# Performance work log

Hardware: AMD Instinct MI355X
Metric: run time of the kernel (lower is better)

## Reference

```python
import jax, jax.numpy as jnp
import numpy as np

N_NODES = 100000


def _gcn_conv(x, edge_index, W, b, n_nodes):
    # GCNConv: add self-loops, symmetric degree normalization, then
    # out[dst] += norm * (x @ W)[src], plus bias.
    src, dst = edge_index[0], edge_index[1]
    loops = jnp.arange(n_nodes, dtype=src.dtype)
    src = jnp.concatenate([src, loops])
    dst = jnp.concatenate([dst, loops])
    deg = jax.ops.segment_sum(jnp.ones_like(dst, dtype=x.dtype), dst,
                              num_segments=n_nodes)
    dinv = jnp.where(deg > 0, jax.lax.rsqrt(deg), 0.0)
    norm = dinv[src] * dinv[dst]            # [E+N]
    h = x @ W                               # [N, out]  (transform BEFORE gather)
    msg = h[src] * norm[:, None]            # [E+N, out]
    out = jax.ops.segment_sum(msg, dst, num_segments=n_nodes)
    return out + b


def setup_inputs() -> dict:
    key = jax.random.key(0)
    ks = jax.random.split(key, 5)
    x = jax.random.normal(ks[0], (N_NODES, 512), dtype=jnp.float32)
    edge_index = jax.random.randint(ks[1], (2, 3200000), 0, N_NODES, dtype=jnp.int64)
    W1 = jax.random.normal(ks[2], (512, 16), dtype=jnp.float32) * (1.0 / np.sqrt(512))
    b1 = jnp.zeros((16,), dtype=jnp.float32)
    W2 = jax.random.normal(ks[3], (16, 7), dtype=jnp.float32) * (1.0 / np.sqrt(16))
    b2 = jnp.zeros((7,), dtype=jnp.float32)
    return {"x": x, "edge_index": edge_index, "W1": W1, "b1": b1, "W2": W2, "b2": b2}


def reference(x, edge_index, W1, b1, W2, b2):
    n = x.shape[0]
    h = _gcn_conv(x, edge_index, W1, b1, n)
    h = jax.nn.relu(h)
    # F.dropout(training=False) is identity in eval mode
    h = _gcn_conv(h, edge_index, W2, b2, n)
    return jax.nn.log_softmax(h, axis=1)
```

## Files before the change

kernel.cpp:

```cpp
#include <hip/hip_runtime.h>
#include <hip/hip_bf16.h>

#define N_NODES 100000
#define N_EDGES 3200000
#define F_IN    512
#define F_H     16
#define F_OUT   7
#define NB      391
#define GPART   512
#define PER_BLK 6256
#define NTILES  6250
#define CAPB    10240
#define NPAD    (NB * 256)

typedef unsigned int u32;
typedef __attribute__((ext_vector_type(8))) __bf16 bf16x8;
typedef __attribute__((ext_vector_type(4))) float f32x4;

union FragU { uint4 q; bf16x8 v; };

static __device__ __forceinline__ float bflo(u32 u) { return __uint_as_float(u << 16); }
static __device__ __forceinline__ float bfhi(u32 u) { return __uint_as_float(u & 0xFFFF0000u); }
static __device__ __forceinline__ unsigned short f2bf(float f) {
  u32 x = __float_as_uint(f);
  x += 0x7FFF + ((x >> 16) & 1);
  return (unsigned short)(x >> 16);
}
static __device__ __forceinline__ u32 cvt2(float a, float b) {
  u32 r;
  asm("v_cvt_pk_bf16_f32 %0, %1, %2" : "=v"(r) : "v"(a), "v"(b));
  return r;
}

__global__ __launch_bounds__(512) void k_prep(int* __restrict__ gcur,
                                              const float* __restrict__ W1,
                                              uint4* __restrict__ bfragG) {
  int tid = threadIdx.x;
  if (tid < NB) gcur[tid] = tid * CAPB;
  for (int idx = tid; idx < 1024; idx += 512) {
    int kk = idx >> 6, lane = idx & 63;
    int col = lane & 15, g = lane >> 4;
    int k0 = kk * 32 + g * 8;
    uint4 q;
    q.x = cvt2(W1[(k0 + 0) * 16 + col], W1[(k0 + 1) * 16 + col]);
    q.y = cvt2(W1[(k0 + 2) * 16 + col], W1[(k0 + 3) * 16 + col]);
    q.z = cvt2(W1[(k0 + 4) * 16 + col], W1[(k0 + 5) * 16 + col]);
    q.w = cvt2(W1[(k0 + 6) * 16 + col], W1[(k0 + 7) * 16 + col]);
    bfragG[idx] = q;
  }
}

__global__ __launch_bounds__(256) void k_part(const int* __restrict__ src,
                                              const int* __restrict__ dst,
                                              int* __restrict__ gcur,
                                              u32* __restrict__ pairs) {
  __shared__ int h[NB];
  __shared__ int lbase[NB];
  __shared__ int lcur[NB];
  int tid = threadIdx.x, blk = blockIdx.x;
  for (int b = tid; b < NB; b += 256) h[b] = 0;
  __syncthreads();
  int e0 = blk * PER_BLK;
  int n = min(PER_BLK, N_EDGES - e0);
  const int4* s4 = (const int4*)(src + e0);
  const int4* d4 = (const int4*)(dst + e0);
  for (int i = tid; i < (n >> 2); i += 256) {
    int4 d = d4[i];
    atomicAdd(&h[d.x >> 8], 1);
    atomicAdd(&h[d.y >> 8], 1);
    atomicAdd(&h[d.z >> 8], 1);
    atomicAdd(&h[d.w >> 8], 1);
  }
  __syncthreads();
  for (int b = tid; b < NB; b += 256) {
    int c = h[b];
    lbase[b] = c ? atomicAdd(&gcur[b], c) : 0;
    lcur[b] = 0;
  }
  __syncthreads();
  for (int i = tid; i < (n >> 2); i += 256) {
    int4 sv = s4[i];
    int4 dv = d4[i];
    { int b = dv.x >> 8; u32 v = ((u32)(dv.x & 255) << 17) | (u32)sv.x;
      pairs[lbase[b] + atomicAdd(&lcur[b], 1)] = v; }
    { int b = dv.y >> 8; u32 v = ((u32)(dv.y & 255) << 17) | (u32)sv.y;
      pairs[lbase[b] + atomicAdd(&lcur[b], 1)] = v; }
    { int b = dv.z >> 8; u32 v = ((u32)(dv.z & 255) << 17) | (u32)sv.z;
      pairs[lbase[b] + atomicAdd(&lcur[b], 1)] = v; }
    { int b = dv.w >> 8; u32 v = ((u32)(dv.w & 255) << 17) | (u32)sv.w;
      pairs[lbase[b] + atomicAdd(&lcur[b], 1)] = v; }
  }
}

__global__ __launch_bounds__(256) void k_deg(const u32* __restrict__ pairs,
                                             const int* __restrict__ gcur,
                                             int* __restrict__ dega,
                                             int* __restrict__ excla) {
  __shared__ int h[256];
  __shared__ int sc[256];
  int tid = threadIdx.x, b = blockIdx.x;
  h[tid] = 0;
  __syncthreads();
  int base = b * CAPB;
  int cnt = gcur[b] - base;
  for (int k = tid; k < cnt; k += 256)
    atomicAdd(&h[pairs[base + k] >> 17], 1);
  __syncthreads();
  int c = h[tid];
  sc[tid] = c;
  __syncthreads();
  for (int off = 1; off < 256; off <<= 1) {
    int v = (tid >= off) ? sc[tid - off] : 0;
    __syncthreads();
    sc[tid] += v;
    __syncthreads();
  }
  int node = b * 256 + tid;
  dega[node] = c;
  excla[node] = sc[tid] - c;
}

__global__ __launch_bounds__(256) void k_gemm1(const float* __restrict__ x,
                                               const uint4* __restrict__ bfragG,
                                               const int* __restrict__ dega,
                                               unsigned short* __restrict__ h1p) {
  __shared__ __align__(16) char ldsbuf[2][64 * 80];
  int tid = threadIdx.x;
  int blockRow0 = blockIdx.x * 64;

  int r0 = tid >> 3, r1 = r0 + 32, s = tid & 7;
  bool ok1 = (blockRow0 + r1) < N_NODES;
  const float* x0 = x + (size_t)(blockRow0 + r0) * F_IN + s * 4;
  const float* x1 = x + (size_t)(blockRow0 + r1) * F_IN + s * 4;

  int wv = tid >> 6, lane = tid & 63;
  int col = lane & 15, g = lane >> 4;
  int wid = blockIdx.x * 4 + wv;
  int fragRow = wv * 16 + col;

  f32x4 acc = {0.f, 0.f, 0.f, 0.f};

  {
    float4 fA = *(const float4*)(x0);
    float4 fB = ok1 ? *(const float4*)(x1) : make_float4(0.f, 0.f, 0.f, 0.f);
    uint2 qA = {cvt2(fA.x, fA.y), cvt2(fA.z, fA.w)};
    uint2 qB = {cvt2(fB.x, fB.y), cvt2(fB.z, fB.w)};
    *(uint2*)(&ldsbuf[0][r0 * 80 + s * 8]) = qA;
    *(uint2*)(&ldsbuf[0][r1 * 80 + s * 8]) = qB;
  }
  __syncthreads();

#pragma unroll
  for (int kk = 0; kk < 16; kk++) {
    int cur = kk & 1;
    float4 fA, fB;
    if (kk < 15) {
      fA = *(const float4*)(x0 + (kk + 1) * 32);
      fB = ok1 ? *(const float4*)(x1 + (kk + 1) * 32) : make_float4(0.f, 0.f, 0.f, 0.f);
    }
    FragU a, b;
    a.q = *(const uint4*)(&ldsbuf[cur][fragRow * 80 + g * 16]);
    b.q = bfragG[kk * 64 + lane];
    acc = __builtin_amdgcn_mfma_f32_16x16x32_bf16(a.v, b.v, acc, 0, 0, 0);
    if (kk < 15) {
      uint2 qA = {cvt2(fA.x, fA.y), cvt2(fA.z, fA.w)};
      uint2 qB = {cvt2(fB.x, fB.y), cvt2(fB.z, fB.w)};
      *(uint2*)(&ldsbuf[cur ^ 1][r0 * 80 + s * 8]) = qA;
      *(uint2*)(&ldsbuf[cur ^ 1][r1 * 80 + s * 8]) = qB;
    }
    __syncthreads();
  }

#pragma unroll
  for (int r = 0; r < 4; r++) {
    int node = wid * 16 + g * 4 + r;
    if (node < N_NODES) {
      float di = rsqrtf((float)(dega[node] + 1));
      h1p[(size_t)node * F_H + col] = f2bf(di * acc[r]);
    }
  }
}

__global__ __launch_bounds__(512) void k_agg1(const u32* __restrict__ pairs,
                                              const int* __restrict__ gcur,
                                              const int* __restrict__ dega,
                                              const int* __restrict__ excla,
                                              const unsigned short* __restrict__ h1p,
                                              const float* __restrict__ b1,
                                              const float* __restrict__ W2,
                                              unsigned short* __restrict__ gfp) {
  __shared__ u32 col[CAPB];
  __shared__ int exc[256];
  __shared__ int dg[256];
  __shared__ int cur[256];
  int tid = threadIdx.x, b = blockIdx.x;
  if (tid < 256) {
    int node = b * 256 + tid;
    dg[tid] = dega[node];
    exc[tid] = excla[node];
    cur[tid] = 0;
  }
  __syncthreads();
  int base = b * CAPB;
  int cnt = gcur[b] - base;
  for (int k = tid; k < cnt; k += 512) {
    u32 v = pairs[base + k];
    int dl = v >> 17;
    col[exc[dl] + atomicAdd(&cur[dl], 1)] = v & 0x1FFFF;
  }
  __syncthreads();

  int dl = tid >> 1, h = tid & 1;
  int node = b * 256 + dl;
  if (node >= N_NODES) return;
  int s0 = exc[dl], c0 = dg[dl];
  const uint4* hp = (const uint4*)h1p;
  float a[8] = {0.f, 0.f, 0.f, 0.f, 0.f, 0.f, 0.f, 0.f};
  for (int e = s0; e < s0 + c0; e++) {
    uint4 hv = hp[col[e] * 2 + h];
    a[0] += bflo(hv.x); a[1] += bfhi(hv.x);
    a[2] += bflo(hv.y); a[3] += bfhi(hv.y);
    a[4] += bflo(hv.z); a[5] += bfhi(hv.z);
    a[6] += bflo(hv.w); a[7] += bfhi(hv.w);
  }
  {
    uint4 hv = hp[node * 2 + h];
    a[0] += bflo(hv.x); a[1] += bfhi(hv.x);
    a[2] += bflo(hv.y); a[3] += bfhi(hv.y);
    a[4] += bflo(hv.z); a[5] += bfhi(hv.z);
    a[6] += bflo(hv.w); a[7] += bfhi(hv.w);
  }
  float di = rsqrtf((float)(c0 + 1));
  float own[8];
#pragma unroll
  for (int k = 0; k < 8; k++)
    own[k] = fmaxf(di * a[k] + b1[h * 8 + k], 0.f);
  float oth[8];
#pragma unroll
  for (int k = 0; k < 8; k++) oth[k] = __shfl_xor(own[k], 1, 64);
  if (h == 0) {
    float o[7] = {0.f, 0.f, 0.f, 0.f, 0.f, 0.f, 0.f};
#pragma unroll
    for (int k = 0; k < 8; k++)
#pragma unroll
      for (int j = 0; j < 7; j++)
        o[j] += own[k] * W2[k * 7 + j] + oth[k] * W2[(k + 8) * 7 + j];
    uint4 q;
    q.x = cvt2(di * o[0], di * o[1]);
    q.y = cvt2(di * o[2], di * o[3]);
    q.z = cvt2(di * o[4], di * o[5]);
    q.w = cvt2(di * o[6], 0.f);
    ((uint4*)gfp)[node] = q;
  }
}

__global__ __launch_bounds__(512) void k_agg2(const u32* __restrict__ pairs,
                                              const int* __restrict__ gcur,
                                              const int* __restrict__ dega,
                                              const int* __restrict__ excla,
                                              const unsigned short* __restrict__ gfp,
                                              const float* __restrict__ b2,
                                              float* __restrict__ out) {
  __shared__ u32 col[CAPB];
  __shared__ int exc[256];
  __shared__ int dg[256];
  __shared__ int cur[256];
  int tid = threadIdx.x, b = blockIdx.x;
  if (tid < 256) {
    int node = b * 256 + tid;
    dg[tid] = dega[node];
    exc[tid] = excla[node];
    cur[tid] = 0;
  }
  __syncthreads();
  int base = b * CAPB;
  int cnt = gcur[b] - base;
  for (int k = tid; k < cnt; k += 512) {
    u32 v = pairs[base + k];
    int dl = v >> 17;
    col[exc[dl] + atomicAdd(&cur[dl], 1)] = v & 0x1FFFF;
  }
  __syncthreads();

  int dl = tid >> 1, h = tid & 1;
  int node = b * 256 + dl;
  if (node >= N_NODES) return;
  int s0 = exc[dl], c0 = dg[dl];
  const uint4* gp = (const uint4*)gfp;
  float a[7] = {0.f, 0.f, 0.f, 0.f, 0.f, 0.f, 0.f};
  for (int e = s0 + h; e < s0 + c0; e += 2) {
    uint4 gv = gp[col[e]];
    a[0] += bflo(gv.x); a[1] += bfhi(gv.x);
    a[2] += bflo(gv.y); a[3] += bfhi(gv.y);
    a[4] += bflo(gv.z); a[5] += bfhi(gv.z);
    a[6] += bflo(gv.w);
  }
#pragma unroll
  for (int j = 0; j < 7; j++) a[j] += __shfl_xor(a[j], 1, 64);
  if (h == 0) {
    uint4 sv = gp[node];
    a[0] += bflo(sv.x); a[1] += bfhi(sv.x);
    a[2] += bflo(sv.y); a[3] += bfhi(sv.y);
    a[4] += bflo(sv.z); a[5] += bfhi(sv.z);
    a[6] += bflo(sv.w);
    float di = rsqrtf((float)(c0 + 1));
    float v[7];
#pragma unroll
    for (int j = 0; j < 7; j++) v[j] = di * a[j] + b2[j];
    float m = v[0];
#pragma unroll
    for (int j = 1; j < 7; j++) m = fmaxf(m, v[j]);
    float s = 0.f;
#pragma unroll
    for (int j = 0; j < 7; j++) s += __expf(v[j] - m);
    float ls = m + logf(s);
#pragma unroll
    for (int j = 0; j < 7; j++) out[(size_t)node * 7 + j] = v[j] - ls;
  }
}

extern "C" void kernel_launch(void* const* d_in, const int* in_sizes, int n_in,
                              void* d_out, int out_size, void* d_ws, size_t ws_size,
                              hipStream_t stream) {
  const float* x  = (const float*)d_in[0];
  const int*   ei = (const int*)d_in[1];
  const float* W1 = (const float*)d_in[2];
  const float* b1 = (const float*)d_in[3];
  const float* W2 = (const float*)d_in[4];
  const float* b2 = (const float*)d_in[5];
  float* out = (float*)d_out;

  char* base = (char*)d_ws;
  int*   gcur   = (int*)(base + 0);
  uint4* bfragG = (uint4*)(base + 2048);
  int*   dega   = (int*)(base + 18432);
  int*   excla  = (int*)(base + 418816);
  u32*   pairs  = (u32*)(base + 819200);
  unsigned short* h1p = (unsigned short*)(base + 16834560);
  unsigned short* gfp = (unsigned short*)(base + 20034560);

  k_prep <<<1, 512, 0, stream>>>(gcur, W1, bfragG);
  k_part <<<GPART, 256, 0, stream>>>(ei, ei + N_EDGES, gcur, pairs);
  k_deg  <<<NB, 256, 0, stream>>>(pairs, gcur, dega, excla);
  k_gemm1<<<(NTILES + 3) / 4, 256, 0, stream>>>(x, bfragG, dega, h1p);
  k_agg1 <<<NB, 512, 0, stream>>>(pairs, gcur, dega, excla, h1p, b1, W2, gfp);
  k_agg2 <<<NB, 512, 0, stream>>>(pairs, gcur, dega, excla, gfp, b2, out);
}
```

Measured before the change: 137.7 us.

## Merge edge partition and GEMM1 into one launch, defer degree scaling

Combines the edge-partitioning kernel and the x@W1 MFMA GEMM into a single grid where the first blocks partition edges and the rest compute the GEMM. The two independent phases can then run concurrently and one launch is removed. Since the GEMM no longer waits on degrees, it writes unscaled bf16 rows, and the degree kernel rescales each row by rsqrt(deg+1) in place. The cost is an extra read and write of h1 plus a second bf16 rounding.

```diff
diff --git a/kernel.cpp b/kernel.cpp
--- a/kernel.cpp
+++ b/kernel.cpp
@@ -10,6 +10,7 @@
 #define GPART   512
 #define PER_BLK 6256
 #define NTILES  6250
+#define GEMMB   1563
 #define CAPB    10240
 #define NPAD    (NB * 256)
 
@@ -50,83 +51,59 @@
   }
 }
 
-__global__ __launch_bounds__(256) void k_part(const int* __restrict__ src,
-                                              const int* __restrict__ dst,
-                                              int* __restrict__ gcur,
-                                              u32* __restrict__ pairs) {
-  __shared__ int h[NB];
-  __shared__ int lbase[NB];
-  __shared__ int lcur[NB];
-  int tid = threadIdx.x, blk = blockIdx.x;
-  for (int b = tid; b < NB; b += 256) h[b] = 0;
-  __syncthreads();
-  int e0 = blk * PER_BLK;
-  int n = min(PER_BLK, N_EDGES - e0);
-  const int4* s4 = (const int4*)(src + e0);
-  const int4* d4 = (const int4*)(dst + e0);
-  for (int i = tid; i < (n >> 2); i += 256) {
-    int4 d = d4[i];
-    atomicAdd(&h[d.x >> 8], 1);
-    atomicAdd(&h[d.y >> 8], 1);
-    atomicAdd(&h[d.z >> 8], 1);
-    atomicAdd(&h[d.w >> 8], 1);
-  }
-  __syncthreads();
-  for (int b = tid; b < NB; b += 256) {
-    int c = h[b];
-    lbase[b] = c ? atomicAdd(&gcur[b], c) : 0;
-    lcur[b] = 0;
-  }
-  __syncthreads();
-  for (int i = tid; i < (n >> 2); i += 256) {
-    int4 sv = s4[i];
-    int4 dv = d4[i];
-    { int b = dv.x >> 8; u32 v = ((u32)(dv.x & 255) << 17) | (u32)sv.x;
-      pairs[lbase[b] + atomicAdd(&lcur[b], 1)] = v; }
-    { int b = dv.y >> 8; u32 v = ((u32)(dv.y & 255) << 17) | (u32)sv.y;
-      pairs[lbase[b] + atomicAdd(&lcur[b], 1)] = v; }
-    { int b = dv.z >> 8; u32 v = ((u32)(dv.z & 255) << 17) | (u32)sv.z;
-      pairs[lbase[b] + atomicAdd(&lcur[b], 1)] = v; }
-    { int b = dv.w >> 8; u32 v = ((u32)(dv.w & 255) << 17) | (u32)sv.w;
-      pairs[lbase[b] + atomicAdd(&lcur[b], 1)] = v; }
-  }
-}
-
-__global__ __launch_bounds__(256) void k_deg(const u32* __restrict__ pairs,
-                                             const int* __restrict__ gcur,
-                                             int* __restrict__ dega,
-                                             int* __restrict__ excla) {
-  __shared__ int h[256];
-  __shared__ int sc[256];
-  int tid = threadIdx.x, b = blockIdx.x;
-  h[tid] = 0;
-  __syncthreads();
-  int base = b * CAPB;
-  int cnt = gcur[b] - base;
-  for (int k = tid; k < cnt; k += 256)
-    atomicAdd(&h[pairs[base + k] >> 17], 1);
-  __syncthreads();
-  int c = h[tid];
-  sc[tid] = c;
-  __syncthreads();
-  for (int off = 1; off < 256; off <<= 1) {
-    int v = (tid >= off) ? sc[tid - off] : 0;
-    __syncthreads();
-    sc[tid] += v;
-    __syncthreads();
-  }
-  int node = b * 256 + tid;
-  dega[node] = c;
-  excla[node] = sc[tid] - c;
-}
-
-__global__ __launch_bounds__(256) void k_gemm1(const float* __restrict__ x,
-                                               const uint4* __restrict__ bfragG,
-                                               const int* __restrict__ dega,
-                                               unsigned short* __restrict__ h1p) {
-  __shared__ __align__(16) char ldsbuf[2][64 * 80];
+__global__ __launch_bounds__(256) void k_pg(const int* __restrict__ src,
+                                            const int* __restrict__ dst,
+                                            int* __restrict__ gcur,
+                                            u32* __restrict__ pairs,
+                                            const float* __restrict__ x,
+                                            const uint4* __restrict__ bfragG,
+                                            unsigned short* __restrict__ h1p) {
+  __shared__ __align__(16) char smem[10240];
   int tid = threadIdx.x;
-  int blockRow0 = blockIdx.x * 64;
+
+  if (blockIdx.x < GPART) {
+    int* h     = (int*)smem;
+    int* lbase = (int*)(smem + 1792);
+    int* lcur  = (int*)(smem + 3584);
+    int blk = blockIdx.x;
+    for (int b = tid; b < NB; b += 256) h[b] = 0;
+    __syncthreads();
+    int e0 = blk * PER_BLK;
+    int n = min(PER_BLK, N_EDGES - e0);
+    const int4* s4 = (const int4*)(src + e0);
+    const int4* d4 = (const int4*)(dst + e0);
+    for (int i = tid; i < (n >> 2); i += 256) {
+      int4 d = d4[i];
+      atomicAdd(&h[d.x >> 8], 1);
+      atomicAdd(&h[d.y >> 8], 1);
+      atomicAdd(&h[d.z >> 8], 1);
+      atomicAdd(&h[d.w >> 8], 1);
+    }
+    __syncthreads();
+    for (int b = tid; b < NB; b += 256) {
+      int c = h[b];
+      lbase[b] = c ? atomicAdd(&gcur[b], c) : 0;
+      lcur[b] = 0;
+    }
+    __syncthreads();
+    for (int i = tid; i < (n >> 2); i += 256) {
+      int4 sv = s4[i];
+      int4 dv = d4[i];
+      { int b = dv.x >> 8; u32 v = ((u32)(dv.x & 255) << 17) | (u32)sv.x;
+        pairs[lbase[b] + atomicAdd(&lcur[b], 1)] = v; }
+      { int b = dv.y >> 8; u32 v = ((u32)(dv.y & 255) << 17) | (u32)sv.y;
+        pairs[lbase[b] + atomicAdd(&lcur[b], 1)] = v; }
+      { int b = dv.z >> 8; u32 v = ((u32)(dv.z & 255) << 17) | (u32)sv.z;
+        pairs[lbase[b] + atomicAdd(&lcur[b], 1)] = v; }
+      { int b = dv.w >> 8; u32 v = ((u32)(dv.w & 255) << 17) | (u32)sv.w;
+        pairs[lbase[b] + atomicAdd(&lcur[b], 1)] = v; }
+    }
+    return;
+  }
+
+  char (*ldsbuf)[64 * 80] = (char (*)[64 * 80])smem;
+  int gb = blockIdx.x - GPART;
+  int blockRow0 = gb * 64;
 
   int r0 = tid >> 3, r1 = r0 + 32, s = tid & 7;
   bool ok1 = (blockRow0 + r1) < N_NODES;
@@ -135,7 +112,7 @@
 
   int wv = tid >> 6, lane = tid & 63;
   int col = lane & 15, g = lane >> 4;
-  int wid = blockIdx.x * 4 + wv;
+  int wid = gb * 4 + wv;
   int fragRow = wv * 16 + col;
 
   f32x4 acc = {0.f, 0.f, 0.f, 0.f};
@@ -174,10 +151,51 @@
 #pragma unroll
   for (int r = 0; r < 4; r++) {
     int node = wid * 16 + g * 4 + r;
-    if (node < N_NODES) {
-      float di = rsqrtf((float)(dega[node] + 1));
-      h1p[(size_t)node * F_H + col] = f2bf(di * acc[r]);
-    }
+    if (node < N_NODES) h1p[(size_t)node * F_H + col] = f2bf(acc[r]);
+  }
+}
+
+__global__ __launch_bounds__(256) void k_deg(const u32* __restrict__ pairs,
+                                             const int* __restrict__ gcur,
+                                             int* __restrict__ dega,
+                                             int* __restrict__ excla,
+                                             unsigned short* __restrict__ h1p) {
+  __shared__ int h[256];
+  __shared__ int sc[256];
+  int tid = threadIdx.x, b = blockIdx.x;
+  h[tid] = 0;
+  __syncthreads();
+  int base = b * CAPB;
+  int cnt = gcur[b] - base;
+  for (int k = tid; k < cnt; k += 256)
+    atomicAdd(&h[pairs[base + k] >> 17], 1);
+  __syncthreads();
+  int c = h[tid];
+  sc[tid] = c;
+  __syncthreads();
+  for (int off = 1; off < 256; off <<= 1) {
+    int v = (tid >= off) ? sc[tid - off] : 0;
+    __syncthreads();
+    sc[tid] += v;
+    __syncthreads();
+  }
+  int node = b * 256 + tid;
+  dega[node] = c;
+  excla[node] = sc[tid] - c;
+  if (node < N_NODES) {
+    float di = rsqrtf((float)(c + 1));
+    uint4* hp4 = (uint4*)h1p;
+    uint4 q0 = hp4[node * 2], q1 = hp4[node * 2 + 1];
+    q0.x = cvt2(di * bflo(q0.x), di * bfhi(q0.x));
+    q0.y = cvt2(di * bflo(q0.y), di * bfhi(q0.y));
+    q0.z = cvt2(di * bflo(q0.z), di * bfhi(q0.z));
+    q0.w = cvt2(di * bflo(q0.w), di * bfhi(q0.w));
+    q1.x = cvt2(di * bflo(q1.x), di * bfhi(q1.x));
+    q1.y = cvt2(di * bflo(q1.y), di * bfhi(q1.y));
+    q1.z = cvt2(di * bflo(q1.z), di * bfhi(q1.z));
+    q1.w = cvt2(di * bflo(q1.w), di * bfhi(q1.w));
+    hp4[node * 2] = q0;
+    hp4[node * 2 + 1] = q1;
   }
 }
 
@@ -339,10 +357,9 @@
   unsigned short* h1p = (unsigned short*)(base + 16834560);
   unsigned short* gfp = (unsigned short*)(base + 20034560);
 
-  k_prep <<<1, 512, 0, stream>>>(gcur, W1, bfragG);
-  k_part <<<GPART, 256, 0, stream>>>(ei, ei + N_EDGES, gcur, pairs);
-  k_deg  <<<NB, 256, 0, stream>>>(pairs, gcur, dega, excla);
-  k_gemm1<<<(NTILES + 3) / 4, 256, 0, stream>>>(x, bfragG, dega, h1p);
-  k_agg1 <<<NB, 512, 0, stream>>>(pairs, gcur, dega, excla, h1p, b1, W2, gfp);
-  k_agg2 <<<NB, 512, 0, stream>>>(pairs, gcur, dega, excla, gfp, b2, out);
-}
+  k_prep<<<1, 512, 0, stream>>>(gcur, W1, bfragG);
+  k_pg  <<<GPART + GEMMB, 256, 0, stream>>>(ei, ei + N_EDGES, gcur, pairs, x, bfragG, h1p);
+  k_deg <<<NB, 256, 0, stream>>>(pairs, gcur, dega, excla, h1p);
+  k_agg1<<<NB, 512, 0, stream>>>(pairs, gcur, dega, excla, h1p, b1, W2, gfp);
+  k_agg2<<<NB, 512, 0, stream>>>(pairs, gcur, dega, excla, gfp, b2, out);
+}
```

Result: no change. 140.4 us (+1.9%).

## Replace global-atomic bucket partition with fixed per-block segments

Applied to the files above, without the earlier changes.

Removes the histogram pass and global atomic offset reservation in the edge partition kernel by giving each (bucket, block) pair a fixed 64-entry segment and storing per-segment counts. Degree and aggregation kernels then walk the segments per thread instead of reading a contiguous bucket. This trades one pass over dst and global atomics for strided, less coalesced reads downstream and a fixed segment capacity that could overflow on skewed inputs.

```diff
diff --git a/kernel.cpp b/kernel.cpp
--- a/kernel.cpp
+++ b/kernel.cpp
@@ -10,7 +10,7 @@
 #define GPART   512
 #define PER_BLK 6256
 #define NTILES  6250
-#define CAPB    10240
+#define CAPSEG  64
 #define NPAD    (NB * 256)
 
 typedef unsigned int u32;
@@ -32,11 +32,9 @@
   return r;
 }
 
-__global__ __launch_bounds__(512) void k_prep(int* __restrict__ gcur,
-                                              const float* __restrict__ W1,
+__global__ __launch_bounds__(512) void k_prep(const float* __restrict__ W1,
                                               uint4* __restrict__ bfragG) {
   int tid = threadIdx.x;
-  if (tid < NB) gcur[tid] = tid * CAPB;
   for (int idx = tid; idx < 1024; idx += 512) {
     int kk = idx >> 6, lane = idx & 63;
     int col = lane & 15, g = lane >> 4;
@@ -52,48 +50,38 @@
 
 __global__ __launch_bounds__(256) void k_part(const int* __restrict__ src,
                                               const int* __restrict__ dst,
-                                              int* __restrict__ gcur,
+                                              int* __restrict__ scnt,
                                               u32* __restrict__ pairs) {
-  __shared__ int h[NB];
-  __shared__ int lbase[NB];
   __shared__ int lcur[NB];
   int tid = threadIdx.x, blk = blockIdx.x;
-  for (int b = tid; b < NB; b += 256) h[b] = 0;
+  for (int b = tid; b < NB; b += 256) lcur[b] = 0;
   __syncthreads();
   int e0 = blk * PER_BLK;
   int n = min(PER_BLK, N_EDGES - e0);
   const int4* s4 = (const int4*)(src + e0);
   const int4* d4 = (const int4*)(dst + e0);
   for (int i = tid; i < (n >> 2); i += 256) {
-    int4 d = d4[i];
-    atomicAdd(&h[d.x >> 8], 1);
-    atomicAdd(&h[d.y >> 8], 1);
-    atomicAdd(&h[d.z >> 8], 1);
-    atomicAdd(&h[d.w >> 8], 1);
-  }
-  __syncthreads();
-  for (int b = tid; b < NB; b += 256) {
-    int c = h[b];
-    lbase[b] = c ? atomicAdd(&gcur[b], c) : 0;
-    lcur[b] = 0;
-  }
-  __syncthreads();
-  for (int i = tid; i < (n >> 2); i += 256) {
     int4 sv = s4[i];
     int4 dv = d4[i];
     { int b = dv.x >> 8; u32 v = ((u32)(dv.x & 255) << 17) | (u32)sv.x;
-      pairs[lbase[b] + atomicAdd(&lcur[b], 1)] = v; }
+      int idx = atomicAdd(&lcur[b], 1);
+      pairs[((size_t)b * GPART + blk) * CAPSEG + idx] = v; }
     { int b = dv.y >> 8; u32 v = ((u32)(dv.y & 255) << 17) | (u32)sv.y;
-      pairs[lbase[b] + atomicAdd(&lcur[b], 1)] = v; }
+      int idx = atomicAdd(&lcur[b], 1);
+      pairs[((size_t)b * GPART + blk) * CAPSEG + idx] = v; }
     { int b = dv.z >> 8; u32 v = ((u32)(dv.z & 255) << 17) | (u32)sv.z;
-      pairs[lbase[b] + atomicAdd(&lcur[b], 1)] = v; }
+      int idx = atomicAdd(&lcur[b], 1);
+      pairs[((size_t)b * GPART + blk) * CAPSEG + idx] = v; }
     { int b = dv.w >> 8; u32 v = ((u32)(dv.w & 255) << 17) | (u32)sv.w;
-      pairs[lbase[b] + atomicAdd(&lcur[b], 1)] = v; }
-  }
+      int idx = atomicAdd(&lcur[b], 1);
+      pairs[((size_t)b * GPART + blk) * CAPSEG + idx] = v; }
+  }
+  __syncthreads();
+  for (int b = tid; b < NB; b += 256) scnt[b * GPART + blk] = lcur[b];
 }
 
 __global__ __launch_bounds__(256) void k_deg(const u32* __restrict__ pairs,
-                                             const int* __restrict__ gcur,
+                                             const int* __restrict__ scnt,
                                              int* __restrict__ dega,
                                              int* __restrict__ excla) {
   __shared__ int h[256];
@@ -101,10 +89,12 @@
   int tid = threadIdx.x, b = blockIdx.x;
   h[tid] = 0;
   __syncthreads();
-  int base = b * CAPB;
-  int cnt = gcur[b] - base;
-  for (int k = tid; k < cnt; k += 256)
-    atomicAdd(&h[pairs[base + k] >> 17], 1);
+  for (int s = tid; s < GPART; s += 256) {
+    int c = scnt[b * GPART + s];
+    const u32* p = pairs + ((size_t)b * GPART + s) * CAPSEG;
+    for (int k = 0; k < c; k++)
+      atomicAdd(&h[p[k] >> 17], 1);
+  }
   __syncthreads();
   int c = h[tid];
   sc[tid] = c;
@@ -182,14 +172,14 @@
 }
 
 __global__ __launch_bounds__(512) void k_agg1(const u32* __restrict__ pairs,
-                                              const int* __restrict__ gcur,
+                                              const int* __restrict__ scnt,
                                               const int* __restrict__ dega,
                                               const int* __restrict__ excla,
                                               const unsigned short* __restrict__ h1p,
                                               const float* __restrict__ b1,
                                               const float* __restrict__ W2,
                                               unsigned short* __restrict__ gfp) {
-  __shared__ u32 col[CAPB];
+  __shared__ u32 col[GPART * 24];
   __shared__ int exc[256];
   __shared__ int dg[256];
   __shared__ int cur[256];
@@ -201,12 +191,14 @@
     cur[tid] = 0;
   }
   __syncthreads();
-  int base = b * CAPB;
-  int cnt = gcur[b] - base;
-  for (int k = tid; k < cnt; k += 512) {
-    u32 v = pairs[base + k];
-    int dl = v >> 17;
-    col[exc[dl] + atomicAdd(&cur[dl], 1)] = v & 0x1FFFF;
+  for (int s = tid; s < GPART; s += 512) {
+    int c = scnt[b * GPART + s];
+    const u32* p = pairs + ((size_t)b * GPART + s) * CAPSEG;
+    for (int k = 0; k < c; k++) {
+      u32 v = p[k];
+      int dl = v >> 17;
+      col[exc[dl] + atomicAdd(&cur[dl], 1)] = v & 0x1FFFF;
+    }
   }
   __syncthreads();
 
@@ -255,13 +247,13 @@
 }
 
 __global__ __launch_bounds__(512) void k_agg2(const u32* __restrict__ pairs,
-                                              const int* __restrict__ gcur,
+                                              const int* __restrict__ scnt,
                                               const int* __restrict__ dega,
                                               const int* __restrict__ excla,
                                               const unsigned short* __restrict__ gfp,
                                               const float* __restrict__ b2,
                                               float* __restrict__ out) {
-  __shared__ u32 col[CAPB];
+  __shared__ u32 col[GPART * 24];
   __shared__ int exc[256];
   __shared__ int dg[256];
   __shared__ int cur[256];
@@ -273,12 +265,14 @@
     cur[tid] = 0;
   }
   __syncthreads();
-  int base = b * CAPB;
-  int cnt = gcur[b] - base;
-  for (int k = tid; k < cnt; k += 512) {
-    u32 v = pairs[base + k];
-    int dl = v >> 17;
-    col[exc[dl] + atomicAdd(&cur[dl], 1)] = v & 0x1FFFF;
+  for (int s = tid; s < GPART; s += 512) {
+    int c = scnt[b * GPART + s];
+    const u32* p = pairs + ((size_t)b * GPART + s) * CAPSEG;
+    for (int k = 0; k < c; k++) {
+      u32 v = p[k];
+      int dl = v >> 17;
+      col[exc[dl] + atomicAdd(&cur[dl], 1)] = v & 0x1FFFF;
+    }
   }
   __syncthreads();
 
@@ -331,18 +325,18 @@
   float* out = (float*)d_out;
 
   char* base = (char*)d_ws;
-  int*   gcur   = (int*)(base + 0);
-  uint4* bfragG = (uint4*)(base + 2048);
-  int*   dega   = (int*)(base + 18432);
-  int*   excla  = (int*)(base + 418816);
-  u32*   pairs  = (u32*)(base + 819200);
-  unsigned short* h1p = (unsigned short*)(base + 16834560);
-  unsigned short* gfp = (unsigned short*)(base + 20034560);
-
-  k_prep <<<1, 512, 0, stream>>>(gcur, W1, bfragG);
-  k_part <<<GPART, 256, 0, stream>>>(ei, ei + N_EDGES, gcur, pairs);
-  k_deg  <<<NB, 256, 0, stream>>>(pairs, gcur, dega, excla);
+  uint4* bfragG = (uint4*)(base + 0);
+  int*   dega   = (int*)(base + 16384);
+  int*   excla  = (int*)(base + 416768);
+  int*   scnt   = (int*)(base + 817152);
+  u32*   pairs  = (u32*)(base + 1617920);
+  unsigned short* h1p = (unsigned short*)(base + 52867072);
+  unsigned short* gfp = (unsigned short*)(base + 56067072);
+
+  k_prep <<<1, 512, 0, stream>>>(W1, bfragG);
+  k_part <<<GPART, 256, 0, stream>>>(ei, ei + N_EDGES, scnt, pairs);
+  k_deg  <<<NB, 256, 0, stream>>>(pairs, scnt, dega, excla);
   k_gemm1<<<(NTILES + 3) / 4, 256, 0, stream>>>(x, bfragG, dega, h1p);
-  k_agg1 <<<NB, 512, 0, stream>>>(pairs, gcur, dega, excla, h1p, b1, W2, gfp);
-  k_agg2 <<<NB, 512, 0, stream>>>(pairs, gcur, dega, excla, gfp, b2, out);
-}
+  k_agg1 <<<NB, 512, 0, stream>>>(pairs, scnt, dega, excla, h1p, b1, W2, gfp);
+  k_agg2 <<<NB, 512, 0, stream>>>(pairs, scnt, dega, excla, gfp, b2, out);
+}
```

After: 146.0 us. 1.06x slower.

## Stage full x row-tile in LDS up front instead of double-buffered k-loop

Applied to the files above, without the earlier changes.

The GEMM1 kernel now loads the entire 64x512 fp32 tile of x into LDS as bf16 in one batched phase, issuing 8 float4 loads at a time, then runs all 16 MFMA steps without per-step barriers. This is meant to raise memory-level parallelism for the bandwidth-bound read of x and remove 16 __syncthreads. In exchange the LDS footprint grows to about 70 KB per block, and launch_bounds(256,2) is set to cap occupancy at two blocks. Out-of-range rows now read row 0 instead of zeros, which only affects outputs that are never stored.

```diff
diff --git a/kernel.cpp b/kernel.cpp
--- a/kernel.cpp
+++ b/kernel.cpp
@@ -12,6 +12,7 @@
 #define NTILES  6250
 #define CAPB    10240
 #define NPAD    (NB * 256)
+#define XPAD    1104
 
 typedef unsigned int u32;
 typedef __attribute__((ext_vector_type(8))) __bf16 bf16x8;
@@ -120,18 +121,37 @@
   excla[node] = sc[tid] - c;
 }
 
-__global__ __launch_bounds__(256) void k_gemm1(const float* __restrict__ x,
-                                               const uint4* __restrict__ bfragG,
-                                               const int* __restrict__ dega,
-                                               unsigned short* __restrict__ h1p) {
-  __shared__ __align__(16) char ldsbuf[2][64 * 80];
+__global__ __launch_bounds__(256, 2) void k_gemm1(const float* __restrict__ x,
+                                                  const uint4* __restrict__ bfragG,
+                                                  const int* __restrict__ dega,
+                                                  unsigned short* __restrict__ h1p) {
+  __shared__ __align__(16) char xt[64 * XPAD];
   int tid = threadIdx.x;
   int blockRow0 = blockIdx.x * 64;
 
   int r0 = tid >> 3, r1 = r0 + 32, s = tid & 7;
   bool ok1 = (blockRow0 + r1) < N_NODES;
-  const float* x0 = x + (size_t)(blockRow0 + r0) * F_IN + s * 4;
-  const float* x1 = x + (size_t)(blockRow0 + r1) * F_IN + s * 4;
+  const float4* x0 = (const float4*)(x + (size_t)(blockRow0 + r0) * F_IN) + s;
+  const float4* x1 = (const float4*)(x + (size_t)(ok1 ? (blockRow0 + r1) : 0) * F_IN) + s;
+
+#pragma unroll
+  for (int t = 0; t < 4; t++) {
+    float4 a0 = x0[(t * 4 + 0) * 8], b0 = x1[(t * 4 + 0) * 8];
+    float4 a1 = x0[(t * 4 + 1) * 8], b1 = x1[(t * 4 + 1) * 8];
+    float4 a2 = x0[(t * 4 + 2) * 8], b2 = x1[(t * 4 + 2) * 8];
+    float4 a3 = x0[(t * 4 + 3) * 8], b3 = x1[(t * 4 + 3) * 8];
+#pragma unroll
+    for (int c = 0; c < 4; c++) {
+      float4 av = (c == 0) ? a0 : (c == 1) ? a1 : (c == 2) ? a2 : a3;
+      float4 bv = (c == 0) ? b0 : (c == 1) ? b1 : (c == 2) ? b2 : b3;
+      int kk = t * 4 + c;
+      uint2 qA = {cvt2(av.x, av.y), cvt2(av.z, av.w)};
+      uint2 qB = {cvt2(bv.x, bv.y), cvt2(bv.z, bv.w)};
+      *(uint2*)(&xt[r0 * XPAD + kk * 64 + s * 8]) = qA;
+      *(uint2*)(&xt[r1 * XPAD + kk * 64 + s * 8]) = qB;
+    }
+  }
+  __syncthreads();
 
   int wv = tid >> 6, lane = tid & 63;
   int col = lane & 15, g = lane >> 4;
@@ -139,36 +159,12 @@
   int fragRow = wv * 16 + col;
 
   f32x4 acc = {0.f, 0.f, 0.f, 0.f};
-
-  {
-    float4 fA = *(const float4*)(x0);
-    float4 fB = ok1 ? *(const float4*)(x1) : make_float4(0.f, 0.f, 0.f, 0.f);
-    uint2 qA = {cvt2(fA.x, fA.y), cvt2(fA.z, fA.w)};
-    uint2 qB = {cvt2(fB.x, fB.y), cvt2(fB.z, fB.w)};
-    *(uint2*)(&ldsbuf[0][r0 * 80 + s * 8]) = qA;
-    *(uint2*)(&ldsbuf[0][r1 * 80 + s * 8]) = qB;
-  }
-  __syncthreads();
-
 #pragma unroll
   for (int kk = 0; kk < 16; kk++) {
-    int cur = kk & 1;
-    float4 fA, fB;
-    if (kk < 15) {
-      fA = *(const float4*)(x0 + (kk + 1) * 32);
-      fB = ok1 ? *(const float4*)(x1 + (kk + 1) * 32) : make_float4(0.f, 0.f, 0.f, 0.f);
-    }
     FragU a, b;
-    a.q = *(const uint4*)(&ldsbuf[cur][fragRow * 80 + g * 16]);
+    a.q = *(const uint4*)(&xt[fragRow * XPAD + kk * 64 + g * 16]);
     b.q = bfragG[kk * 64 + lane];
     acc = __builtin_amdgcn_mfma_f32_16x16x32_bf16(a.v, b.v, acc, 0, 0, 0);
-    if (kk < 15) {
-      uint2 qA = {cvt2(fA.x, fA.y), cvt2(fA.z, fA.w)};
-      uint2 qB = {cvt2(fB.x, fB.y), cvt2(fB.z, fB.w)};
-      *(uint2*)(&ldsbuf[cur ^ 1][r0 * 80 + s * 8]) = qA;
-      *(uint2*)(&ldsbuf[cur ^ 1][r1 * 80 + s * 8]) = qB;
-    }
-    __syncthreads();
   }
 
 #pragma unroll
```

Result: slower. 146.1 us (+6.1%).
